# Optimization experiments

Hardware: AMD Instinct MI355X
Metric: run time of the kernel (lower is better)

The kernel has to match this reference:

```python
import jax, jax.numpy as jnp
import numpy as np

D_MODEL = 1024
N_HEADS = 16
HEAD_DIM = D_MODEL // N_HEADS
EPS = 1e-6


def setup_inputs() -> dict:
    key = jax.random.key(0)
    k1, k2, k3 = jax.random.split(key, 3)
    b, l, d = 2, 2048, D_MODEL
    x = jax.random.normal(k1, (b, l, d), dtype=jnp.float32)
    # Linear weights stored so that y = x @ W (no bias), matching torch math
    w_qkv = jax.random.normal(k2, (d, 3 * d), dtype=jnp.float32) * (1.0 / np.sqrt(d))
    w_proj = jax.random.normal(k3, (d, d), dtype=jnp.float32) * (1.0 / np.sqrt(d))
    norm_w = jnp.ones((d,), dtype=jnp.float32)
    return {"x": x, "norm_w": norm_w, "w_qkv": w_qkv, "w_proj": w_proj}


def rms_norm(x, w, eps=EPS):
    x32 = x.astype(jnp.float32)
    inv_rms = jax.lax.rsqrt(jnp.mean(x32 * x32, axis=-1, keepdims=True) + eps)
    return (x32 * inv_rms).astype(x.dtype) * w.astype(x.dtype)


def reference(x, norm_w, w_qkv, w_proj):
    b, l, d = x.shape
    h = rms_norm(x, norm_w)
    qkv = h @ w_qkv                       # [b, l, 3d]
    q, k, v = jnp.split(qkv, 3, axis=-1)

    def heads(t):
        return t.reshape(b, l, N_HEADS, HEAD_DIM).transpose(0, 2, 1, 3)  # [b,h,l,hd]

    q, k, v = heads(q), heads(k), heads(v)
    scale = 1.0 / np.sqrt(HEAD_DIM)
    scores = jnp.einsum('bhqd,bhkd->bhqk', q, k) * scale  # full LxL scores
    attn = jax.nn.softmax(scores, axis=-1)
    ctx = jnp.einsum('bhqk,bhkd->bhqd', attn, v)
    ctx = ctx.transpose(0, 2, 1, 3).reshape(b, l, d)
    out = ctx @ w_proj
    return x + out
```

## Files before the change

kernel.cpp:

```cpp
#include <hip/hip_runtime.h>
#include <hip/hip_bf16.h>
#include <cstdint>
#include <cstddef>

typedef __attribute__((ext_vector_type(8))) short bf16x8;
typedef __attribute__((ext_vector_type(4))) float f32x4;
typedef __attribute__((ext_vector_type(16))) float f32x16;

#define GLD_LDS16(gptr, lptr)                                                  \
  __builtin_amdgcn_global_load_lds(                                            \
      (const __attribute__((address_space(1))) void*)(gptr),                   \
      (__attribute__((address_space(3))) void*)(lptr), 16, 0, 0)

__device__ __forceinline__ uint32_t cvtpk(float a, float b) {
  uint32_t d;
  asm("v_cvt_pk_bf16_f32 %0, %1, %2" : "=v"(d) : "v"(a), "v"(b));
  return d;
}

__device__ __forceinline__ float xhalf_sum(float x) {
  auto r = __builtin_amdgcn_permlane32_swap(__float_as_uint(x),
                                            __float_as_uint(x), false, false);
  return __uint_as_float(r[0]) + __uint_as_float(r[1]);
}

__global__ __launch_bounds__(256) void rmsnorm_kernel(
    const float* __restrict__ x, const float* __restrict__ w,
    __hip_bfloat16* __restrict__ h) {
  const int row = blockIdx.x;
  const int tid = threadIdx.x;
  const float4 v = reinterpret_cast<const float4*>(x + (size_t)row * 1024)[tid];
  float ss = v.x * v.x + v.y * v.y + v.z * v.z + v.w * v.w;
#pragma unroll
  for (int off = 32; off >= 1; off >>= 1) ss += __shfl_down(ss, off);
  __shared__ float red[4];
  if ((tid & 63) == 0) red[tid >> 6] = ss;
  __syncthreads();
  const float inv =
      rsqrtf((red[0] + red[1] + red[2] + red[3]) * (1.0f / 1024.0f) + 1e-6f);
  const float4 wv = reinterpret_cast<const float4*>(w)[tid];
  __hip_bfloat16* hp = h + (size_t)row * 1024 + tid * 4;
  hp[0] = __float2bfloat16(v.x * inv * wv.x);
  hp[1] = __float2bfloat16(v.y * inv * wv.y);
  hp[2] = __float2bfloat16(v.z * inv * wv.z);
  hp[3] = __float2bfloat16(v.w * inv * wv.w);
}

__global__ __launch_bounds__(256) void transpose_cast2_kernel(
    const float* __restrict__ w_qkv, const float* __restrict__ w_proj,
    __hip_bfloat16* __restrict__ wqkvT, __hip_bfloat16* __restrict__ wprojT) {
  __shared__ float tile[32][33];
  const float* src;
  __hip_bfloat16* dst;
  int C, bx;
  if (blockIdx.x < 96) {
    src = w_qkv; dst = wqkvT; C = 3072; bx = blockIdx.x * 32;
  } else {
    src = w_proj; dst = wprojT; C = 1024; bx = (blockIdx.x - 96) * 32;
  }
  const int R = 1024;
  const int by = blockIdx.y * 32;
  const int tx = threadIdx.x;
  const int ty = threadIdx.y;
#pragma unroll
  for (int j = 0; j < 32; j += 8)
    tile[ty + j][tx] = src[(size_t)(by + ty + j) * C + bx + tx];
  __syncthreads();
#pragma unroll
  for (int j = 0; j < 32; j += 8)
    dst[(size_t)(bx + ty + j) * R + by + tx] = __float2bfloat16(tile[tx][ty + j]);
}

template <int BM, int BN, int RESID>
__device__ __forceinline__ void gemm_tile(
    const __hip_bfloat16* __restrict__ A, const __hip_bfloat16* __restrict__ BT,
    void* __restrict__ Cout, const float* __restrict__ resid, int M, int N,
    int K, int bx, int by, __hip_bfloat16* As, __hip_bfloat16* Bs) {
  const int tid = threadIdx.x;
  const int lane = tid & 63;
  const int wid = tid >> 6;
  const int m0 = by * BM;
  const int n0 = bx * BN;
  const int wr = wid >> 1, wc = wid & 1;
  constexpr int MI = BM / 32, NJ = BN / 32;
  constexpr int NCHA = BM / 16, NCHB = BN / 16;
  f32x4 acc[MI][NJ] = {};
  const int nk = K >> 5;
  const int lr = lane & 15, lk = lane >> 4;
  for (int kt = 0; kt < nk; ++kt) {
#pragma unroll
    for (int it = 0; it < NCHA / 4; ++it) {
      const int c = wid + it * 4;
      const int e = c * 512 + lane * 8;
      GLD_LDS16(A + (size_t)(m0 + (e >> 5)) * K + kt * 32 + (e & 31),
                As + c * 512);
    }
#pragma unroll
    for (int it = 0; it < NCHB / 4; ++it) {
      const int c = wid + it * 4;
      const int e = c * 512 + lane * 8;
      GLD_LDS16(BT + (size_t)(n0 + (e >> 5)) * K + kt * 32 + (e & 31),
                Bs + c * 512);
    }
    __syncthreads();
    bf16x8 af[MI], bfr[NJ];
#pragma unroll
    for (int i = 0; i < MI; ++i)
      af[i] = *(const bf16x8*)(As + (wr * (BM / 2) + i * 16 + lr) * 32 + lk * 8);
#pragma unroll
    for (int j = 0; j < NJ; ++j)
      bfr[j] = *(const bf16x8*)(Bs + (wc * (BN / 2) + j * 16 + lr) * 32 + lk * 8);
#pragma unroll
    for (int i = 0; i < MI; ++i)
#pragma unroll
      for (int j = 0; j < NJ; ++j)
        acc[i][j] = __builtin_amdgcn_mfma_f32_16x16x32_bf16(af[i], bfr[j],
                                                            acc[i][j], 0, 0, 0);
    __syncthreads();
  }
#pragma unroll
  for (int i = 0; i < MI; ++i)
#pragma unroll
    for (int j = 0; j < NJ; ++j)
#pragma unroll
      for (int r = 0; r < 4; ++r) {
        const int row = m0 + wr * (BM / 2) + i * 16 + lk * 4 + r;
        const int col = n0 + wc * (BN / 2) + j * 16 + lr;
        const float v = acc[i][j][r];
        if (RESID) {
          ((float*)Cout)[(size_t)row * N + col] =
              resid[(size_t)row * N + col] + v;
        } else {
          ((__hip_bfloat16*)Cout)[(size_t)row * N + col] = __float2bfloat16(v);
        }
      }
}

__global__ __launch_bounds__(256) void qkv_gemm_kernel(
    const __hip_bfloat16* __restrict__ h, const __hip_bfloat16* __restrict__ wqkT,
    const __hip_bfloat16* __restrict__ wvT, __hip_bfloat16* __restrict__ qkbuf,
    __hip_bfloat16* __restrict__ vTbuf) {
  __shared__ __align__(16) __hip_bfloat16 As[128 * 32];
  __shared__ __align__(16) __hip_bfloat16 Bs[128 * 32];
  const int bid = blockIdx.x;
  if (bid < 512) {
    const int xcd = bid & 7, seq = bid >> 3;
    const int by = (xcd >> 1) * 8 + (seq >> 3);
    const int bx = (xcd & 1) * 8 + (seq & 7);
    gemm_tile<128, 128, 0>(h, wqkT, (void*)qkbuf, nullptr, 4096, 2048, 1024,
                           bx, by, As, Bs);
  } else {
    const int t = bid - 512;
    const int xcd = t & 7, seq = t >> 3;
    const int by = seq >> 2;
    const int bx = xcd * 4 + (seq & 3);
    gemm_tile<128, 128, 0>(wvT, h, (void*)vTbuf, nullptr, 1024, 4096, 1024, bx,
                           by, As, Bs);
  }
}

__global__ __launch_bounds__(256) void proj_gemm_kernel(
    const __hip_bfloat16* __restrict__ ctx, const __hip_bfloat16* __restrict__ wpT,
    float* __restrict__ out, const float* __restrict__ x) {
  __shared__ __align__(16) __hip_bfloat16 As[128 * 32];
  __shared__ __align__(16) __hip_bfloat16 Bs[64 * 32];
  const int bid = blockIdx.x;
  const int xcd = bid & 7, seq = bid >> 3;
  const int by = xcd * 4 + (seq >> 4);
  const int bx = seq & 15;
  gemm_tile<128, 64, 1>(ctx, wpT, (void*)out, x, 4096, 1024, 1024, bx, by, As,
                        Bs);
}

__global__ __launch_bounds__(256, 2) void attn_kernel(
    const __hip_bfloat16* __restrict__ qk, const __hip_bfloat16* __restrict__ vT,
    __hip_bfloat16* __restrict__ ctx) {
  const int flat = blockIdx.x;
  const int xcd = flat & 7, seq = flat >> 3;
  const int bh = xcd * 4 + (seq >> 4);
  const int qt = seq & 15;
  const int b = bh >> 4, h = bh & 15;
  const int tid = threadIdx.x, lane = tid & 63, wid = tid >> 6;
  const size_t tok0 = (size_t)b * 2048;
  const int q0 = qt * 128 + wid * 32;
  const int l31 = lane & 31;
  const int hi = lane >> 5;

  __shared__ __align__(16) char Kl[2][64 * 128];
  __shared__ __align__(16) char Vl[2][64 * 128];

  const int sr = tid >> 2;
  const int scB = (tid & 3) * 32;
  const int swW = (sr & 7) << 4;
  const int wA = sr * 128 + (scB ^ swW);
  const int wB = sr * 128 + ((scB + 16) ^ swW);

  const __hip_bfloat16* kbase = qk + tok0 * 2048 + 1024 + (size_t)h * 64;
  const __hip_bfloat16* vbase = vT + ((size_t)(h * 64 + sr)) * 4096 + tok0;
  const int scE = (tid & 3) * 16;

  bf16x8 qf[4];
  {
    const __hip_bfloat16* qptr = qk + (tok0 + q0 + l31) * 2048 + h * 64 + hi * 8;
    const float c = 0.125f * 1.44269504f;
#pragma unroll
    for (int ks = 0; ks < 4; ++ks) {
      bf16x8 v = *(const bf16x8*)(qptr + ks * 16);
      const __hip_bfloat16* ie = (const __hip_bfloat16*)&v;
      __hip_bfloat16* oe = (__hip_bfloat16*)&qf[ks];
#pragma unroll
      for (int i = 0; i < 8; ++i)
        oe[i] = __float2bfloat16(__bfloat162float(ie[i]) * c);
    }
  }

  const int swR = (l31 & 7) << 4;
  const int rb0 = l31 * 128;
  const int rb1 = (32 + l31) * 128;

  bf16x8 kreg0, kreg1, vreg0, vreg1;
  auto load_tile = [&](int t) {
    const __hip_bfloat16* kp = kbase + (size_t)(t * 64 + sr) * 2048 + scE;
    kreg0 = *(const bf16x8*)kp;
    kreg1 = *(const bf16x8*)(kp + 8);
    const __hip_bfloat16* vp = vbase + t * 64 + scE;
    vreg0 = *(const bf16x8*)vp;
    vreg1 = *(const bf16x8*)(vp + 8);
  };
  auto write_tile = [&](int bf) {
    *(bf16x8*)(Kl[bf] + wA) = kreg0;
    *(bf16x8*)(Kl[bf] + wB) = kreg1;
    *(bf16x8*)(Vl[bf] + wA) = vreg0;
    *(bf16x8*)(Vl[bf] + wB) = vreg1;
  };

  f32x16 oT0 = {}, oT1 = {};
  float lacc = 0.f;

  load_tile(0);
  write_tile(0);
  __syncthreads();

  for (int kvt = 0; kvt < 32; ++kvt) {
    const int cur = kvt & 1;
    if (kvt + 1 < 32) load_tile(kvt + 1);

    f32x16 s0 = {}, s1 = {};
    __builtin_amdgcn_s_setprio(1);
#pragma unroll
    for (int ks = 0; ks < 4; ++ks) {
      const int cOff = (ks * 32 + hi * 16) ^ swR;
      const bf16x8 kf0 = *(const bf16x8*)(Kl[cur] + rb0 + cOff);
      const bf16x8 kf1 = *(const bf16x8*)(Kl[cur] + rb1 + cOff);
      s0 = __builtin_amdgcn_mfma_f32_32x32x16_bf16(kf0, qf[ks], s0, 0, 0, 0);
      s1 = __builtin_amdgcn_mfma_f32_32x32x16_bf16(kf1, qf[ks], s1, 0, 0, 0);
    }
    __builtin_amdgcn_s_setprio(0);

    float ps = 0.f;
    uint32_t pk0[8], pk1[8];
#pragma unroll
    for (int i = 0; i < 8; ++i) {
      const float a0 = __builtin_amdgcn_exp2f(s0[2 * i]);
      const float a1 = __builtin_amdgcn_exp2f(s0[2 * i + 1]);
      const float b0 = __builtin_amdgcn_exp2f(s1[2 * i]);
      const float b1 = __builtin_amdgcn_exp2f(s1[2 * i + 1]);
      ps += (a0 + a1) + (b0 + b1);
      pk0[i] = cvtpk(a0, a1);
      pk1[i] = cvtpk(b0, b1);
    }
    lacc += ps;

#pragma unroll
    for (int ts = 0; ts < 4; ++ts) {
      const uint32_t* pk = (ts < 2) ? pk0 : pk1;
      const int o = (ts & 1) * 4;
      auto w02 = __builtin_amdgcn_permlane32_swap(pk[o], pk[o + 2], false, false);
      auto w13 =
          __builtin_amdgcn_permlane32_swap(pk[o + 1], pk[o + 3], false, false);
      uint32_t fr[4] = {w02[0], w13[0], w02[1], w13[1]};
      const bf16x8 pf = *(const bf16x8*)fr;
      const int cOff = (ts * 32 + hi * 16) ^ swR;
      const bf16x8 vf0 = *(const bf16x8*)(Vl[cur] + rb0 + cOff);
      const bf16x8 vf1 = *(const bf16x8*)(Vl[cur] + rb1 + cOff);
      __builtin_amdgcn_s_setprio(1);
      oT0 = __builtin_amdgcn_mfma_f32_32x32x16_bf16(vf0, pf, oT0, 0, 0, 0);
      oT1 = __builtin_amdgcn_mfma_f32_32x32x16_bf16(vf1, pf, oT1, 0, 0, 0);
      __builtin_amdgcn_s_setprio(0);
    }

    if (kvt + 1 < 32) write_tile(cur ^ 1);
    __syncthreads();
  }

  const float lrow = xhalf_sum(lacc);
  const float linv = 1.0f / lrow;
  __hip_bfloat16* cb = ctx + (tok0 + q0 + l31) * 1024 + h * 64;
#pragma unroll
  for (int dh = 0; dh < 2; ++dh) {
#pragma unroll
    for (int rq = 0; rq < 4; ++rq) {
      const int d0 = 8 * rq + 4 * hi + 32 * dh;
      float v0, v1, v2, v3;
      if (dh) {
        v0 = oT1[4 * rq];
        v1 = oT1[4 * rq + 1];
        v2 = oT1[4 * rq + 2];
        v3 = oT1[4 * rq + 3];
      } else {
        v0 = oT0[4 * rq];
        v1 = oT0[4 * rq + 1];
        v2 = oT0[4 * rq + 2];
        v3 = oT0[4 * rq + 3];
      }
      *(uint32_t*)(cb + d0) = cvtpk(v0 * linv, v1 * linv);
      *(uint32_t*)(cb + d0 + 2) = cvtpk(v2 * linv, v3 * linv);
    }
  }
}

extern "C" void kernel_launch(void* const* d_in, const int* in_sizes, int n_in,
                              void* d_out, int out_size, void* d_ws,
                              size_t ws_size, hipStream_t stream) {
  const float* x = (const float*)d_in[0];
  const float* norm_w = (const float*)d_in[1];
  const float* w_qkv = (const float*)d_in[2];
  const float* w_proj = (const float*)d_in[3];
  float* out = (float*)d_out;

  char* ws = (char*)d_ws;
  __hip_bfloat16* hbuf = (__hip_bfloat16*)(ws);
  __hip_bfloat16* wqkvT = (__hip_bfloat16*)(ws + (size_t)8 * 1024 * 1024);
  __hip_bfloat16* wprojT = (__hip_bfloat16*)(ws + (size_t)14 * 1024 * 1024);
  __hip_bfloat16* qkbuf = (__hip_bfloat16*)(ws + (size_t)16 * 1024 * 1024);
  __hip_bfloat16* vTbuf = (__hip_bfloat16*)(ws + (size_t)32 * 1024 * 1024);
  __hip_bfloat16* ctx = (__hip_bfloat16*)(ws + (size_t)40 * 1024 * 1024);

  rmsnorm_kernel<<<dim3(4096), dim3(256), 0, stream>>>(x, norm_w, hbuf);
  transpose_cast2_kernel<<<dim3(128, 32), dim3(32, 8), 0, stream>>>(
      w_qkv, w_proj, wqkvT, wprojT);
  qkv_gemm_kernel<<<dim3(768), dim3(256), 0, stream>>>(
      hbuf, wqkvT, wqkvT + (size_t)2048 * 1024, qkbuf, vTbuf);
  attn_kernel<<<dim3(512), dim3(256), 0, stream>>>(qkbuf, vTbuf, ctx);
  proj_gemm_kernel<<<dim3(512), dim3(256), 0, stream>>>(ctx, wprojT, out, x);
}
```

Baseline: 110.6 us.

## Software-pipeline attention loop: overlap next QK^T with current PV using triple-buffered LDS

New measurement: 110.0 us. About the same (-0.5%).

```diff
diff --git a/kernel.cpp b/kernel.cpp
--- a/kernel.cpp
+++ b/kernel.cpp
@@ -186,8 +186,8 @@
   const int l31 = lane & 31;
   const int hi = lane >> 5;
 
-  __shared__ __align__(16) char Kl[2][64 * 128];
-  __shared__ __align__(16) char Vl[2][64 * 128];
+  __shared__ __align__(16) char Kl[3][64 * 128];
+  __shared__ __align__(16) char Vl[3][64 * 128];
 
   const int sr = tid >> 2;
   const int scB = (tid & 3) * 32;
@@ -233,30 +233,29 @@
     *(bf16x8*)(Vl[bf] + wA) = vreg0;
     *(bf16x8*)(Vl[bf] + wB) = vreg1;
   };
+  auto qk_tile = [&](int bf, f32x16& d0, f32x16& d1) {
+#pragma unroll
+    for (int ks = 0; ks < 4; ++ks) {
+      const int cOff = (ks * 32 + hi * 16) ^ swR;
+      const bf16x8 kf0 = *(const bf16x8*)(Kl[bf] + rb0 + cOff);
+      const bf16x8 kf1 = *(const bf16x8*)(Kl[bf] + rb1 + cOff);
+      d0 = __builtin_amdgcn_mfma_f32_32x32x16_bf16(kf0, qf[ks], d0, 0, 0, 0);
+      d1 = __builtin_amdgcn_mfma_f32_32x32x16_bf16(kf1, qf[ks], d1, 0, 0, 0);
+    }
+  };
 
   f32x16 oT0 = {}, oT1 = {};
   float lacc = 0.f;
 
   load_tile(0);
   write_tile(0);
+  load_tile(1);
   __syncthreads();
-
-  for (int kvt = 0; kvt < 32; ++kvt) {
-    const int cur = kvt & 1;
-    if (kvt + 1 < 32) load_tile(kvt + 1);
-
-    f32x16 s0 = {}, s1 = {};
-    __builtin_amdgcn_s_setprio(1);
-#pragma unroll
-    for (int ks = 0; ks < 4; ++ks) {
-      const int cOff = (ks * 32 + hi * 16) ^ swR;
-      const bf16x8 kf0 = *(const bf16x8*)(Kl[cur] + rb0 + cOff);
-      const bf16x8 kf1 = *(const bf16x8*)(Kl[cur] + rb1 + cOff);
-      s0 = __builtin_amdgcn_mfma_f32_32x32x16_bf16(kf0, qf[ks], s0, 0, 0, 0);
-      s1 = __builtin_amdgcn_mfma_f32_32x32x16_bf16(kf1, qf[ks], s1, 0, 0, 0);
-    }
-    __builtin_amdgcn_s_setprio(0);
-
+  f32x16 s0 = {}, s1 = {};
+  qk_tile(0, s0, s1);
+
+  int bcur = 0, bnext = 1, bnn = 2;
+  for (int t = 0; t < 32; ++t) {
     float ps = 0.f;
     uint32_t pk0[8], pk1[8];
 #pragma unroll
@@ -270,6 +269,14 @@
       pk1[i] = cvtpk(b0, b1);
     }
     lacc += ps;
+
+    if (t + 1 < 32) write_tile(bnext);
+    if (t + 2 < 32) load_tile(t + 2);
+    __syncthreads();
+
+    __builtin_amdgcn_s_setprio(1);
+    f32x16 ns0 = {}, ns1 = {};
+    if (t + 1 < 32) qk_tile(bnext, ns0, ns1);
 
 #pragma unroll
     for (int ts = 0; ts < 4; ++ts) {
@@ -281,16 +288,19 @@
       uint32_t fr[4] = {w02[0], w13[0], w02[1], w13[1]};
       const bf16x8 pf = *(const bf16x8*)fr;
       const int cOff = (ts * 32 + hi * 16) ^ swR;
-      const bf16x8 vf0 = *(const bf16x8*)(Vl[cur] + rb0 + cOff);
-      const bf16x8 vf1 = *(const bf16x8*)(Vl[cur] + rb1 + cOff);
-      __builtin_amdgcn_s_setprio(1);
+      const bf16x8 vf0 = *(const bf16x8*)(Vl[bcur] + rb0 + cOff);
+      const bf16x8 vf1 = *(const bf16x8*)(Vl[bcur] + rb1 + cOff);
       oT0 = __builtin_amdgcn_mfma_f32_32x32x16_bf16(vf0, pf, oT0, 0, 0, 0);
       oT1 = __builtin_amdgcn_mfma_f32_32x32x16_bf16(vf1, pf, oT1, 0, 0, 0);
-      __builtin_amdgcn_s_setprio(0);
-    }
-
-    if (kvt + 1 < 32) write_tile(cur ^ 1);
-    __syncthreads();
+    }
+    __builtin_amdgcn_s_setprio(0);
+
+    s0 = ns0;
+    s1 = ns1;
+    const int tmp = bcur;
+    bcur = bnext;
+    bnext = bnn;
+    bnn = tmp;
   }
 
   const float lrow = xhalf_sum(lacc);
```

## Double GEMM K-step to 64 and give each attention wave 64 query rows

Applied to the files above, without the earlier changes.

Measured after the change: 126.8 us. 1.15x slower.

```diff
diff --git a/kernel.cpp b/kernel.cpp
--- a/kernel.cpp
+++ b/kernel.cpp
@@ -83,39 +83,48 @@
   const int n0 = bx * BN;
   const int wr = wid >> 1, wc = wid & 1;
   constexpr int MI = BM / 32, NJ = BN / 32;
-  constexpr int NCHA = BM / 16, NCHB = BN / 16;
   f32x4 acc[MI][NJ] = {};
-  const int nk = K >> 5;
+  const int nk = K >> 6;
   const int lr = lane & 15, lk = lane >> 4;
+  const int srow = lane >> 2;
+  const int scol = (lane & 3) * 8;
   for (int kt = 0; kt < nk; ++kt) {
 #pragma unroll
-    for (int it = 0; it < NCHA / 4; ++it) {
+    for (int it = 0; it < BM / 32; ++it) {
       const int c = wid + it * 4;
-      const int e = c * 512 + lane * 8;
-      GLD_LDS16(A + (size_t)(m0 + (e >> 5)) * K + kt * 32 + (e & 31),
+      const int sub = c / (BM / 16), cc = c % (BM / 16);
+      GLD_LDS16(A + (size_t)(m0 + cc * 16 + srow) * K + kt * 64 + sub * 32 + scol,
                 As + c * 512);
     }
 #pragma unroll
-    for (int it = 0; it < NCHB / 4; ++it) {
+    for (int it = 0; it < BN / 32; ++it) {
       const int c = wid + it * 4;
-      const int e = c * 512 + lane * 8;
-      GLD_LDS16(BT + (size_t)(n0 + (e >> 5)) * K + kt * 32 + (e & 31),
+      const int sub = c / (BN / 16), cc = c % (BN / 16);
+      GLD_LDS16(BT + (size_t)(n0 + cc * 16 + srow) * K + kt * 64 + sub * 32 + scol,
                 Bs + c * 512);
     }
     __syncthreads();
-    bf16x8 af[MI], bfr[NJ];
+    bf16x8 af[MI][2], bfr[NJ][2];
 #pragma unroll
     for (int i = 0; i < MI; ++i)
-      af[i] = *(const bf16x8*)(As + (wr * (BM / 2) + i * 16 + lr) * 32 + lk * 8);
+#pragma unroll
+      for (int s = 0; s < 2; ++s)
+        af[i][s] = *(const bf16x8*)(As + s * (BM * 32) +
+                                    (wr * (BM / 2) + i * 16 + lr) * 32 + lk * 8);
 #pragma unroll
     for (int j = 0; j < NJ; ++j)
-      bfr[j] = *(const bf16x8*)(Bs + (wc * (BN / 2) + j * 16 + lr) * 32 + lk * 8);
-#pragma unroll
-    for (int i = 0; i < MI; ++i)
-#pragma unroll
-      for (int j = 0; j < NJ; ++j)
-        acc[i][j] = __builtin_amdgcn_mfma_f32_16x16x32_bf16(af[i], bfr[j],
-                                                            acc[i][j], 0, 0, 0);
+#pragma unroll
+      for (int s = 0; s < 2; ++s)
+        bfr[j][s] = *(const bf16x8*)(Bs + s * (BN * 32) +
+                                     (wc * (BN / 2) + j * 16 + lr) * 32 + lk * 8);
+#pragma unroll
+    for (int s = 0; s < 2; ++s)
+#pragma unroll
+      for (int i = 0; i < MI; ++i)
+#pragma unroll
+        for (int j = 0; j < NJ; ++j)
+          acc[i][j] = __builtin_amdgcn_mfma_f32_16x16x32_bf16(
+              af[i][s], bfr[j][s], acc[i][j], 0, 0, 0);
     __syncthreads();
   }
 #pragma unroll
@@ -140,8 +149,8 @@
     const __hip_bfloat16* __restrict__ h, const __hip_bfloat16* __restrict__ wqkT,
     const __hip_bfloat16* __restrict__ wvT, __hip_bfloat16* __restrict__ qkbuf,
     __hip_bfloat16* __restrict__ vTbuf) {
-  __shared__ __align__(16) __hip_bfloat16 As[128 * 32];
-  __shared__ __align__(16) __hip_bfloat16 Bs[128 * 32];
+  __shared__ __align__(16) __hip_bfloat16 As[128 * 64];
+  __shared__ __align__(16) __hip_bfloat16 Bs[128 * 64];
   const int bid = blockIdx.x;
   if (bid < 512) {
     const int xcd = bid & 7, seq = bid >> 3;
@@ -162,8 +171,8 @@
 __global__ __launch_bounds__(256) void proj_gemm_kernel(
     const __hip_bfloat16* __restrict__ ctx, const __hip_bfloat16* __restrict__ wpT,
     float* __restrict__ out, const float* __restrict__ x) {
-  __shared__ __align__(16) __hip_bfloat16 As[128 * 32];
-  __shared__ __align__(16) __hip_bfloat16 Bs[64 * 32];
+  __shared__ __align__(16) __hip_bfloat16 As[128 * 64];
+  __shared__ __align__(16) __hip_bfloat16 Bs[64 * 64];
   const int bid = blockIdx.x;
   const int xcd = bid & 7, seq = bid >> 3;
   const int by = xcd * 4 + (seq >> 4);
@@ -172,7 +181,7 @@
                         Bs);
 }
 
-__global__ __launch_bounds__(256, 2) void attn_kernel(
+__global__ __launch_bounds__(128) void attn_kernel(
     const __hip_bfloat16* __restrict__ qk, const __hip_bfloat16* __restrict__ vT,
     __hip_bfloat16* __restrict__ ctx) {
   const int flat = blockIdx.x;
@@ -182,35 +191,40 @@
   const int b = bh >> 4, h = bh & 15;
   const int tid = threadIdx.x, lane = tid & 63, wid = tid >> 6;
   const size_t tok0 = (size_t)b * 2048;
-  const int q0 = qt * 128 + wid * 32;
+  const int q0 = qt * 128 + wid * 64;
   const int l31 = lane & 31;
   const int hi = lane >> 5;
 
   __shared__ __align__(16) char Kl[2][64 * 128];
   __shared__ __align__(16) char Vl[2][64 * 128];
 
-  const int sr = tid >> 2;
-  const int scB = (tid & 3) * 32;
+  const int sr = tid >> 1;
+  const int scE = (tid & 1) * 32;
+  const int scB = (tid & 1) * 64;
   const int swW = (sr & 7) << 4;
-  const int wA = sr * 128 + (scB ^ swW);
-  const int wB = sr * 128 + ((scB + 16) ^ swW);
 
   const __hip_bfloat16* kbase = qk + tok0 * 2048 + 1024 + (size_t)h * 64;
   const __hip_bfloat16* vbase = vT + ((size_t)(h * 64 + sr)) * 4096 + tok0;
-  const int scE = (tid & 3) * 16;
-
-  bf16x8 qf[4];
+
+  bf16x8 qfA[4], qfB[4];
   {
-    const __hip_bfloat16* qptr = qk + (tok0 + q0 + l31) * 2048 + h * 64 + hi * 8;
     const float c = 0.125f * 1.44269504f;
+    const __hip_bfloat16* qA = qk + (tok0 + q0 + l31) * 2048 + h * 64 + hi * 8;
+    const __hip_bfloat16* qB =
+        qk + (tok0 + q0 + 32 + l31) * 2048 + h * 64 + hi * 8;
 #pragma unroll
     for (int ks = 0; ks < 4; ++ks) {
-      bf16x8 v = *(const bf16x8*)(qptr + ks * 16);
-      const __hip_bfloat16* ie = (const __hip_bfloat16*)&v;
-      __hip_bfloat16* oe = (__hip_bfloat16*)&qf[ks];
-#pragma unroll
-      for (int i = 0; i < 8; ++i)
-        oe[i] = __float2bfloat16(__bfloat162float(ie[i]) * c);
+      bf16x8 va = *(const bf16x8*)(qA + ks * 16);
+      bf16x8 vb = *(const bf16x8*)(qB + ks * 16);
+      const __hip_bfloat16* ia = (const __hip_bfloat16*)&va;
+      const __hip_bfloat16* ib = (const __hip_bfloat16*)&vb;
+      __hip_bfloat16* oa = (__hip_bfloat16*)&qfA[ks];
+      __hip_bfloat16* ob = (__hip_bfloat16*)&qfB[ks];
+#pragma unroll
+      for (int i = 0; i < 8; ++i) {
+        oa[i] = __float2bfloat16(__bfloat162float(ia[i]) * c);
+        ob[i] = __float2bfloat16(__bfloat162float(ib[i]) * c);
+      }
     }
   }
 
@@ -218,24 +232,26 @@
   const int rb0 = l31 * 128;
   const int rb1 = (32 + l31) * 128;
 
-  bf16x8 kreg0, kreg1, vreg0, vreg1;
+  bf16x8 kr[4], vr[4];
   auto load_tile = [&](int t) {
     const __hip_bfloat16* kp = kbase + (size_t)(t * 64 + sr) * 2048 + scE;
-    kreg0 = *(const bf16x8*)kp;
-    kreg1 = *(const bf16x8*)(kp + 8);
     const __hip_bfloat16* vp = vbase + t * 64 + scE;
-    vreg0 = *(const bf16x8*)vp;
-    vreg1 = *(const bf16x8*)(vp + 8);
+#pragma unroll
+    for (int k = 0; k < 4; ++k) kr[k] = *(const bf16x8*)(kp + 8 * k);
+#pragma unroll
+    for (int k = 0; k < 4; ++k) vr[k] = *(const bf16x8*)(vp + 8 * k);
   };
   auto write_tile = [&](int bf) {
-    *(bf16x8*)(Kl[bf] + wA) = kreg0;
-    *(bf16x8*)(Kl[bf] + wB) = kreg1;
-    *(bf16x8*)(Vl[bf] + wA) = vreg0;
-    *(bf16x8*)(Vl[bf] + wB) = vreg1;
+#pragma unroll
+    for (int k = 0; k < 4; ++k) {
+      const int off = sr * 128 + ((scB + 16 * k) ^ swW);
+      *(bf16x8*)(Kl[bf] + off) = kr[k];
+      *(bf16x8*)(Vl[bf] + off) = vr[k];
+    }
   };
 
-  f32x16 oT0 = {}, oT1 = {};
-  float lacc = 0.f;
+  f32x16 oA0 = {}, oA1 = {}, oB0 = {}, oB1 = {};
+  float lA = 0.f, lB = 0.f;
 
   load_tile(0);
   write_tile(0);
@@ -245,76 +261,102 @@
     const int cur = kvt & 1;
     if (kvt + 1 < 32) load_tile(kvt + 1);
 
-    f32x16 s0 = {}, s1 = {};
-    __builtin_amdgcn_s_setprio(1);
+    f32x16 sA0 = {}, sA1 = {}, sB0 = {}, sB1 = {};
 #pragma unroll
     for (int ks = 0; ks < 4; ++ks) {
       const int cOff = (ks * 32 + hi * 16) ^ swR;
       const bf16x8 kf0 = *(const bf16x8*)(Kl[cur] + rb0 + cOff);
       const bf16x8 kf1 = *(const bf16x8*)(Kl[cur] + rb1 + cOff);
-      s0 = __builtin_amdgcn_mfma_f32_32x32x16_bf16(kf0, qf[ks], s0, 0, 0, 0);
-      s1 = __builtin_amdgcn_mfma_f32_32x32x16_bf16(kf1, qf[ks], s1, 0, 0, 0);
-    }
-    __builtin_amdgcn_s_setprio(0);
-
-    float ps = 0.f;
-    uint32_t pk0[8], pk1[8];
+      sA0 = __builtin_amdgcn_mfma_f32_32x32x16_bf16(kf0, qfA[ks], sA0, 0, 0, 0);
+      sA1 = __builtin_amdgcn_mfma_f32_32x32x16_bf16(kf1, qfA[ks], sA1, 0, 0, 0);
+      sB0 = __builtin_amdgcn_mfma_f32_32x32x16_bf16(kf0, qfB[ks], sB0, 0, 0, 0);
+      sB1 = __builtin_amdgcn_mfma_f32_32x32x16_bf16(kf1, qfB[ks], sB1, 0, 0, 0);
+    }
+
+    float psA = 0.f, psB = 0.f;
+    uint32_t pA0[8], pA1[8], pB0[8], pB1[8];
 #pragma unroll
     for (int i = 0; i < 8; ++i) {
-      const float a0 = __builtin_amdgcn_exp2f(s0[2 * i]);
-      const float a1 = __builtin_amdgcn_exp2f(s0[2 * i + 1]);
-      const float b0 = __builtin_amdgcn_exp2f(s1[2 * i]);
-      const float b1 = __builtin_amdgcn_exp2f(s1[2 * i + 1]);
-      ps += (a0 + a1) + (b0 + b1);
-      pk0[i] = cvtpk(a0, a1);
-      pk1[i] = cvtpk(b0, b1);
-    }
-    lacc += ps;
+      const float a0 = __builtin_amdgcn_exp2f(sA0[2 * i]);
+      const float a1 = __builtin_amdgcn_exp2f(sA0[2 * i + 1]);
+      const float a2 = __builtin_amdgcn_exp2f(sA1[2 * i]);
+      const float a3 = __builtin_amdgcn_exp2f(sA1[2 * i + 1]);
+      psA += (a0 + a1) + (a2 + a3);
+      pA0[i] = cvtpk(a0, a1);
+      pA1[i] = cvtpk(a2, a3);
+      const float b0 = __builtin_amdgcn_exp2f(sB0[2 * i]);
+      const float b1 = __builtin_amdgcn_exp2f(sB0[2 * i + 1]);
+      const float b2 = __builtin_amdgcn_exp2f(sB1[2 * i]);
+      const float b3 = __builtin_amdgcn_exp2f(sB1[2 * i + 1]);
+      psB += (b0 + b1) + (b2 + b3);
+      pB0[i] = cvtpk(b0, b1);
+      pB1[i] = cvtpk(b2, b3);
+    }
+    lA += psA;
+    lB += psB;
 
 #pragma unroll
     for (int ts = 0; ts < 4; ++ts) {
-      const uint32_t* pk = (ts < 2) ? pk0 : pk1;
-      const int o = (ts & 1) * 4;
-      auto w02 = __builtin_amdgcn_permlane32_swap(pk[o], pk[o + 2], false, false);
-      auto w13 =
-          __builtin_amdgcn_permlane32_swap(pk[o + 1], pk[o + 3], false, false);
-      uint32_t fr[4] = {w02[0], w13[0], w02[1], w13[1]};
-      const bf16x8 pf = *(const bf16x8*)fr;
       const int cOff = (ts * 32 + hi * 16) ^ swR;
       const bf16x8 vf0 = *(const bf16x8*)(Vl[cur] + rb0 + cOff);
       const bf16x8 vf1 = *(const bf16x8*)(Vl[cur] + rb1 + cOff);
-      __builtin_amdgcn_s_setprio(1);
-      oT0 = __builtin_amdgcn_mfma_f32_32x32x16_bf16(vf0, pf, oT0, 0, 0, 0);
-      oT1 = __builtin_amdgcn_mfma_f32_32x32x16_bf16(vf1, pf, oT1, 0, 0, 0);
-      __builtin_amdgcn_s_setprio(0);
+      const int o = (ts & 1) * 4;
+      {
+        const uint32_t* pk = (ts < 2) ? pA0 : pA1;
+        auto w02 =
+            __builtin_amdgcn_permlane32_swap(pk[o], pk[o + 2], false, false);
+        auto w13 =
+            __builtin_amdgcn_permlane32_swap(pk[o + 1], pk[o + 3], false, false);
+        uint32_t fr[4] = {w02[0], w13[0], w02[1], w13[1]};
+        const bf16x8 pf = *(const bf16x8*)fr;
+        oA0 = __builtin_amdgcn_mfma_f32_32x32x16_bf16(vf0, pf, oA0, 0, 0, 0);
+        oA1 = __builtin_amdgcn_mfma_f32_32x32x16_bf16(vf1, pf, oA1, 0, 0, 0);
+      }
+      {
+        const uint32_t* pk = (ts < 2) ? pB0 : pB1;
+        auto w02 =
+            __builtin_amdgcn_permlane32_swap(pk[o], pk[o + 2], false, false);
+        auto w13 =
+            __builtin_amdgcn_permlane32_swap(pk[o + 1], pk[o + 3], false, false);
+        uint32_t fr[4] = {w02[0], w13[0], w02[1], w13[1]};
+        const bf16x8 pf = *(const bf16x8*)fr;
+        oB0 = __builtin_amdgcn_mfma_f32_32x32x16_bf16(vf0, pf, oB0, 0, 0, 0);
+        oB1 = __builtin_amdgcn_mfma_f32_32x32x16_bf16(vf1, pf, oB1, 0, 0, 0);
+      }
     }
 
     if (kvt + 1 < 32) write_tile(cur ^ 1);
     __syncthreads();
   }
 
-  const float lrow = xhalf_sum(lacc);
-  const float linv = 1.0f / lrow;
-  __hip_bfloat16* cb = ctx + (tok0 + q0 + l31) * 1024 + h * 64;
-#pragma unroll
-  for (int dh = 0; dh < 2; ++dh) {
-#pragma unroll
-    for (int rq = 0; rq < 4; ++rq) {
-      const int d0 = 8 * rq + 4 * hi + 32 * dh;
-      float v0, v1, v2, v3;
-      if (dh) {
-        v0 = oT1[4 * rq];
-        v1 = oT1[4 * rq + 1];
-        v2 = oT1[4 * rq + 2];
-        v3 = oT1[4 * rq + 3];
-      } else {
-        v0 = oT0[4 * rq];
-        v1 = oT0[4 * rq + 1];
-        v2 = oT0[4 * rq + 2];
-        v3 = oT0[4 * rq + 3];
-      }
-      *(uint32_t*)(cb + d0) = cvtpk(v0 * linv, v1 * linv);
-      *(uint32_t*)(cb + d0 + 2) = cvtpk(v2 * linv, v3 * linv);
+#pragma unroll
+  for (int qb = 0; qb < 2; ++qb) {
+    const float lrow = xhalf_sum(qb ? lB : lA);
+    const float linv = 1.0f / lrow;
+    __hip_bfloat16* cb =
+        ctx + (tok0 + q0 + qb * 32 + l31) * 1024 + h * 64;
+    const f32x16& o0 = qb ? oB0 : oA0;
+    const f32x16& o1 = qb ? oB1 : oA1;
+#pragma unroll
+    for (int dh = 0; dh < 2; ++dh) {
+#pragma unroll
+      for (int rq = 0; rq < 4; ++rq) {
+        const int d0 = 8 * rq + 4 * hi + 32 * dh;
+        float v0, v1, v2, v3;
+        if (dh) {
+          v0 = o1[4 * rq];
+          v1 = o1[4 * rq + 1];
+          v2 = o1[4 * rq + 2];
+          v3 = o1[4 * rq + 3];
+        } else {
+          v0 = o0[4 * rq];
+          v1 = o0[4 * rq + 1];
+          v2 = o0[4 * rq + 2];
+          v3 = o0[4 * rq + 3];
+        }
+        *(uint32_t*)(cb + d0) = cvtpk(v0 * linv, v1 * linv);
+        *(uint32_t*)(cb + d0 + 2) = cvtpk(v2 * linv, v3 * linv);
+      }
     }
   }
 }
@@ -341,6 +383,6 @@
       w_qkv, w_proj, wqkvT, wprojT);
   qkv_gemm_kernel<<<dim3(768), dim3(256), 0, stream>>>(
       hbuf, wqkvT, wqkvT + (size_t)2048 * 1024, qkbuf, vTbuf);
-  attn_kernel<<<dim3(512), dim3(256), 0, stream>>>(qkbuf, vTbuf, ctx);
+  attn_kernel<<<dim3(512), dim3(128), 0, stream>>>(qkbuf, vTbuf, ctx);
   proj_gemm_kernel<<<dim3(512), dim3(256), 0, stream>>>(ctx, wprojT, out, x);
 }
```
